# Kernel tuning notes

Hardware: AMD Instinct MI355X
Metric: run time of the kernel (lower is better)

The kernel has to match this reference:

```python
import jax, jax.numpy as jnp
import numpy as np

B, S, H = 4, 2048, 1024
NH, HD = 16, 64


def setup_inputs() -> dict:
    key = jax.random.key(0)
    ks = jax.random.split(key, 5)
    scale = 1.0 / np.sqrt(H)
    x = jax.random.normal(ks[0], (B, S, H), dtype=jnp.float32)
    w_qkv = jax.random.normal(ks[1], (H, 3 * H), dtype=jnp.float32) * scale
    b_qkv = jnp.zeros((3 * H,), dtype=jnp.float32)
    w_out = jax.random.normal(ks[2], (H, H), dtype=jnp.float32) * scale
    b_out = jnp.zeros((H,), dtype=jnp.float32)
    return {"x": x, "w_qkv": w_qkv, "b_qkv": b_qkv, "w_out": w_out, "b_out": b_out}


def reference(x, w_qkv, b_qkv, w_out, b_out):
    bsz, seq_len, hidden = x.shape
    qkv = x @ w_qkv + b_qkv  # [B,S,3H]
    q, k, v = jnp.split(qkv, 3, axis=-1)

    def heads(t):
        return t.reshape(bsz, seq_len, NH, HD).transpose(0, 2, 1, 3)  # [B,NH,S,HD]

    q, k, v = heads(q), heads(k), heads(v)
    scale = HD ** (-0.5)
    attn = jnp.einsum("bhqd,bhkd->bhqk", q, k) * scale  # [B,NH,S,S]
    causal = jnp.tril(jnp.ones((seq_len, seq_len), dtype=bool))
    attn = jnp.where(causal, attn, -jnp.inf)
    probs = jax.nn.softmax(attn, axis=-1)
    out = jnp.einsum("bhqk,bhkd->bhqd", probs, v)
    out = out.transpose(0, 2, 1, 3).reshape(bsz, seq_len, hidden)
    return out @ w_out + b_out
```

## Files before the change

### kernel.cpp

```cpp
#include <hip/hip_runtime.h>
#include <hip/hip_bf16.h>
#include <cstdint>

#define B_  4
#define S_  2048
#define H_  1024
#define NH_ 16
#define HD_ 64

using short8  = __attribute__((ext_vector_type(8))) short;
using floatx4 = __attribute__((ext_vector_type(4))) float;

__device__ __forceinline__ unsigned short f2b(float f) {
  union { float f; unsigned int u; } x; x.f = f;
  unsigned int r = x.u + 0x7fffu + ((x.u >> 16) & 1u);
  return (unsigned short)(r >> 16);
}
__device__ __forceinline__ unsigned short f2b_fast(float f) {
  union { float f; unsigned int u; } x; x.f = f;
  return (unsigned short)((x.u + 0x8000u) >> 16);
}
__device__ __forceinline__ unsigned int pack2(float a, float b) {
  return (unsigned int)f2b(a) | ((unsigned int)f2b(b) << 16);
}

__device__ __forceinline__ void async16(void* lds, const void* g) {
  __builtin_amdgcn_global_load_lds(
      (const __attribute__((address_space(1))) unsigned int*)g,
      (__attribute__((address_space(3))) unsigned int*)lds, 16, 0, 0);
}

__device__ __forceinline__ void transpose_tile(const float* __restrict__ in,
                                               unsigned short* __restrict__ out,
                                               int R, int C, int c0, int r0) {
  __shared__ float tile[32][33];
  int tx = threadIdx.x & 31, ty = threadIdx.x >> 5;
  for (int i = 0; i < 4; i++) {
    int r = r0 + ty + i * 8;
    tile[ty + i * 8][tx] = in[(size_t)r * C + c0 + tx];
  }
  __syncthreads();
  for (int i = 0; i < 4; i++) {
    int c = c0 + ty + i * 8;
    out[(size_t)c * R + r0 + tx] = f2b(tile[tx][ty + i * 8]);
  }
}

__global__ void k_prep(const float* __restrict__ x, const float* __restrict__ w_qkv,
                       const float* __restrict__ w_out,
                       unsigned short* __restrict__ xb, unsigned short* __restrict__ wqkvT,
                       unsigned short* __restrict__ woutT) {
  int bx = blockIdx.x;
  if (bx < 8192) {
    int i = (bx * 256 + threadIdx.x) * 4;
    float4 v = *(const float4*)(x + i);
    ushort4 o;
    o.x = f2b(v.x); o.y = f2b(v.y); o.z = f2b(v.z); o.w = f2b(v.w);
    *(ushort4*)(xb + i) = o;
  } else if (bx < 8192 + 3072) {
    int t = bx - 8192;
    transpose_tile(w_qkv, wqkvT, H_, 3 * H_, (t % 96) * 32, (t / 96) * 32);
  } else {
    int t = bx - 8192 - 3072;
    transpose_tile(w_out, woutT, H_, H_, (t & 31) * 32, (t >> 5) * 32);
  }
}

template <bool OUT_BF16>
__global__ __launch_bounds__(256, 2) void k_gemm_wide(
    const unsigned short* __restrict__ A,
    const unsigned short* __restrict__ BT,
    const float* __restrict__ bias,
    void* __restrict__ Cout,
    unsigned short* __restrict__ vt,
    int M, int N, int K) {
  __shared__ __align__(16) unsigned short As[2][128 * 32];
  __shared__ __align__(16) unsigned short Bs[2][256 * 32];
  const int tid  = threadIdx.x;
  const int lane = tid & 63, wave = tid >> 6;
  const int quad = lane >> 4, l16 = lane & 15;
  const int wm = wave >> 1, wn = wave & 1;
  const int m0 = blockIdx.y * 128, n0 = blockIdx.x * 256;

  floatx4 acc[4][8];
#pragma unroll
  for (int mt = 0; mt < 4; mt++)
#pragma unroll
    for (int nt = 0; nt < 8; nt++)
      acc[mt][nt] = (floatx4){0.f, 0.f, 0.f, 0.f};

  auto stage = [&](int k0, int bufi) {
#pragma unroll
    for (int j = 0; j < 6; j++) {
      int g = wave * 384 + j * 64 + lane;
      if (g < 512) {
        int row = g >> 2, c8 = (g & 3) ^ ((row >> 1) & 3);
        async16(&As[bufi][g * 8], &A[(size_t)(m0 + row) * K + k0 + c8 * 8]);
      } else {
        int c = g - 512;
        int row = c >> 2, c8 = (c & 3) ^ ((row >> 1) & 3);
        async16(&Bs[bufi][c * 8], &BT[(size_t)(n0 + row) * K + k0 + c8 * 8]);
      }
    }
  };

  stage(0, 0);
  int it = 0;
  for (int k0 = 0; k0 < K; k0 += 32, it++) {
    const int cur = it & 1;
    __syncthreads();
    if (k0 + 32 < K) stage(k0 + 32, cur ^ 1);

    short8 af[4];
#pragma unroll
    for (int t = 0; t < 4; t++) {
      int ra = wm * 64 + t * 16 + l16;
      af[t] = *(const short8*)&As[cur][(ra * 4 + (quad ^ ((ra >> 1) & 3))) * 8];
    }
#pragma unroll
    for (int h = 0; h < 2; h++) {
      short8 bq[4];
#pragma unroll
      for (int t = 0; t < 4; t++) {
        int rb = wn * 128 + (h * 4 + t) * 16 + l16;
        bq[t] = *(const short8*)&Bs[cur][(rb * 4 + (quad ^ ((rb >> 1) & 3))) * 8];
      }
#pragma unroll
      for (int mt = 0; mt < 4; mt++)
#pragma unroll
        for (int nt = 0; nt < 4; nt++)
          acc[mt][h * 4 + nt] =
              __builtin_amdgcn_mfma_f32_16x16x32_bf16(af[mt], bq[nt], acc[mt][h * 4 + nt], 0, 0, 0);
    }
  }

  if (OUT_BF16 && n0 >= 2048) {
#pragma unroll
    for (int mt = 0; mt < 4; mt++) {
      int row0 = m0 + wm * 64 + mt * 16 + quad * 4;
      int b = row0 >> 11, s = row0 & 2047;
#pragma unroll
      for (int nt = 0; nt < 8; nt++) {
        int col = n0 + wn * 128 + nt * 16 + l16;
        float bv = bias[col];
        uint2 u;
        u.x = pack2(acc[mt][nt][0] + bv, acc[mt][nt][1] + bv);
        u.y = pack2(acc[mt][nt][2] + bv, acc[mt][nt][3] + bv);
        *(uint2*)&vt[(size_t)(b * 1024 + (col - 2048)) * S_ + s] = u;
      }
    }
  } else {
#pragma unroll
    for (int mt = 0; mt < 4; mt++) {
      int row = m0 + wm * 64 + mt * 16 + quad * 4;
#pragma unroll
      for (int nt = 0; nt < 8; nt++) {
        int col = n0 + wn * 128 + nt * 16 + l16;
        float bv = bias[col];
#pragma unroll
        for (int r = 0; r < 4; r++) {
          float v = acc[mt][nt][r] + bv;
          if (OUT_BF16) ((unsigned short*)Cout)[(size_t)(row + r) * N + col] = f2b(v);
          else          ((float*)Cout)[(size_t)(row + r) * N + col] = v;
        }
      }
    }
  }
}

template <bool OUT_BF16>
__global__ __launch_bounds__(256, 4) void k_gemm_bt(
    const unsigned short* __restrict__ A,
    const unsigned short* __restrict__ BT,
    const float* __restrict__ bias,
    void* __restrict__ Cout,
    unsigned short* __restrict__ vt,
    int M, int N, int K) {
  __shared__ __align__(16) unsigned short As[2][128 * 32];
  __shared__ __align__(16) unsigned short Bs[2][128 * 32];
  const int tid  = threadIdx.x;
  const int lane = tid & 63, wave = tid >> 6;
  const int quad = lane >> 4, l16 = lane & 15;
  const int wm = wave >> 1, wn = wave & 1;
  const int m0 = blockIdx.y * 128, n0 = blockIdx.x * 128;
  const int wv2 = wave & 1;

  const unsigned short* srcbase = (wave < 2) ? A : BT;
  const int base0 = (wave < 2) ? m0 : n0;

  floatx4 acc[4][4];
  for (int mt = 0; mt < 4; mt++)
    for (int nt = 0; nt < 4; nt++)
      acc[mt][nt] = (floatx4){0.f, 0.f, 0.f, 0.f};

  auto stage = [&](int k0, int bufi) {
    unsigned short* dst = (wave < 2) ? &As[bufi][0] : &Bs[bufi][0];
    for (int j = 0; j < 4; j++) {
      int c = wv2 * 256 + j * 64 + lane;
      int row = c >> 2, slot = c & 3;
      int c8 = slot ^ ((row >> 1) & 3);
      async16(&dst[c * 8], &srcbase[(size_t)(base0 + row) * K + k0 + c8 * 8]);
    }
  };

  stage(0, 0);
  int it = 0;
  for (int k0 = 0; k0 < K; k0 += 32, it++) {
    const int cur = it & 1;
    __syncthreads();
    if (k0 + 32 < K) stage(k0 + 32, cur ^ 1);
    short8 af[4], bq[4];
    for (int t = 0; t < 4; t++) {
      int ra = wm * 64 + t * 16 + l16;
      int rb = wn * 64 + t * 16 + l16;
      af[t] = *(const short8*)&As[cur][(ra * 4 + (quad ^ ((ra >> 1) & 3))) * 8];
      bq[t] = *(const short8*)&Bs[cur][(rb * 4 + (quad ^ ((rb >> 1) & 3))) * 8];
    }
    for (int mt = 0; mt < 4; mt++)
      for (int nt = 0; nt < 4; nt++)
        acc[mt][nt] = __builtin_amdgcn_mfma_f32_16x16x32_bf16(af[mt], bq[nt], acc[mt][nt], 0, 0, 0);
  }

  if (OUT_BF16 && n0 >= 2048) {
    for (int mt = 0; mt < 4; mt++) {
      int row0 = m0 + wm * 64 + mt * 16 + quad * 4;
      int b = row0 >> 11, s = row0 & 2047;
      for (int nt = 0; nt < 4; nt++) {
        int col = n0 + wn * 64 + nt * 16 + l16;
        float bv = bias[col];
        uint2 u;
        u.x = pack2(acc[mt][nt][0] + bv, acc[mt][nt][1] + bv);
        u.y = pack2(acc[mt][nt][2] + bv, acc[mt][nt][3] + bv);
        *(uint2*)&vt[(size_t)(b * 1024 + (col - 2048)) * S_ + s] = u;
      }
    }
  } else {
    for (int mt = 0; mt < 4; mt++) {
      int row = m0 + wm * 64 + mt * 16 + quad * 4;
      for (int nt = 0; nt < 4; nt++) {
        int col = n0 + wn * 64 + nt * 16 + l16;
        float bv = bias[col];
        for (int r = 0; r < 4; r++) {
          float v = acc[mt][nt][r] + bv;
          if (OUT_BF16) ((unsigned short*)Cout)[(size_t)(row + r) * N + col] = f2b(v);
          else          ((float*)Cout)[(size_t)(row + r) * N + col] = v;
        }
      }
    }
  }
}

__global__ __launch_bounds__(256, 3) void k_attn(
    const unsigned short* __restrict__ qkv,
    const unsigned short* __restrict__ vt,
    unsigned short* __restrict__ outb) {
  __shared__ __align__(16) unsigned short Ks [2][64 * 64];
  __shared__ __align__(16) unsigned short VTs[2][64 * 64];
  __shared__ __align__(16) unsigned short Ps[4][16 * 64];

  const int tid  = threadIdx.x;
  const int lane = tid & 63, w = tid >> 6;
  const int quad = lane >> 4, l16 = lane & 15;
  const int qt = (S_ / 128 - 1) - (blockIdx.x >> 6);
  const int bh = blockIdx.x & 63;
  const int b = bh >> 4, h = bh & 15;
  const int qwv = qt * 128 + w * 32;
  const int wv2 = w & 1;

  short8 qf[2][2];
  for (int g = 0; g < 2; g++)
    for (int kh = 0; kh < 2; kh++)
      qf[g][kh] = *(const short8*)&qkv[(size_t)(b * S_ + qwv + g * 16 + l16) * (3 * H_)
                                       + h * HD_ + kh * 32 + quad * 8];

  floatx4 oacc[2][4];
  float lsum[2] = {0.f, 0.f};
  for (int g = 0; g < 2; g++)
    for (int ct = 0; ct < 4; ct++) oacc[g][ct] = (floatx4){0.f, 0.f, 0.f, 0.f};

  auto stage = [&](int kt, int bufi) {
    if (w < 2) {
      for (int j = 0; j < 4; j++) {
        int c = wv2 * 256 + j * 64 + lane;
        int row = c >> 3, c8 = (c & 7) ^ (row & 7);
        async16(&Ks[bufi][c * 8],
                &qkv[(size_t)(b * S_ + kt * 64 + row) * (3 * H_) + H_ + h * HD_ + c8 * 8]);
      }
    } else {
      for (int j = 0; j < 4; j++) {
        int c = wv2 * 256 + j * 64 + lane;
        int row = c >> 3, c8 = (c & 7) ^ (row & 7);
        async16(&VTs[bufi][c * 8],
                &vt[(size_t)(bh * HD_ + row) * S_ + kt * 64 + c8 * 8]);
      }
    }
  };

  unsigned short* Pw = &Ps[w][0];

  const int ktmax = 2 * qt + 1;
  stage(0, 0);
  for (int kt = 0; kt <= ktmax; kt++) {
    const int cur = kt & 1;
    __syncthreads();
    if (kt < ktmax) stage(kt + 1, cur ^ 1);

    if (kt * 64 <= qwv + 31) {
      const bool need_mask = (kt * 64 + 63 > qwv);

      short8 vf[4][2];
      for (int ct = 0; ct < 4; ct++)
        for (int kh = 0; kh < 2; kh++) {
          int vrow = ct * 16 + l16;
          vf[ct][kh] = *(const short8*)&VTs[cur][(vrow * 8 + ((kh * 4 + quad) ^ (vrow & 7))) * 8];
        }

      uint2 pk[2][4];
      for (int ct = 0; ct < 4; ct++) {
        int krow = ct * 16 + l16;
        short8 kf0 = *(const short8*)&Ks[cur][(krow * 8 + ((0 + quad) ^ (krow & 7))) * 8];
        short8 kf1 = *(const short8*)&Ks[cur][(krow * 8 + ((4 + quad) ^ (krow & 7))) * 8];
        for (int g = 0; g < 2; g++) {
          floatx4 z = (floatx4){0.f, 0.f, 0.f, 0.f};
          z = __builtin_amdgcn_mfma_f32_16x16x32_bf16(kf0, qf[g][0], z, 0, 0, 0);
          z = __builtin_amdgcn_mfma_f32_16x16x32_bf16(kf1, qf[g][1], z, 0, 0, 0);
          float p[4];
          if (need_mask) {
            int kvb = kt * 64 + ct * 16 + quad * 4;
            int q = qwv + g * 16 + l16;
            for (int r = 0; r < 4; r++)
              p[r] = (kvb + r <= q) ? __expf(z[r] * 0.125f) : 0.f;
          } else {
            for (int r = 0; r < 4; r++) p[r] = __expf(z[r] * 0.125f);
          }
          lsum[g] += (p[0] + p[1]) + (p[2] + p[3]);
          pk[g][ct].x = (unsigned int)f2b_fast(p[0]) | ((unsigned int)f2b_fast(p[1]) << 16);
          pk[g][ct].y = (unsigned int)f2b_fast(p[2]) | ((unsigned int)f2b_fast(p[3]) << 16);
        }
      }

      for (int g = 0; g < 2; g++) {
        for (int ct = 0; ct < 4; ct++) {
          int slot = (ct * 2 + (quad >> 1)) ^ (l16 & 7);
          *(uint2*)&Pw[l16 * 64 + slot * 8 + (quad & 1) * 4] = pk[g][ct];
        }
        for (int kh = 0; kh < 2; kh++) {
          short8 pf = *(const short8*)&Pw[l16 * 64 + ((kh * 4 + quad) ^ (l16 & 7)) * 8];
          for (int ct = 0; ct < 4; ct++)
            oacc[g][ct] = __builtin_amdgcn_mfma_f32_16x16x32_bf16(vf[ct][kh], pf, oacc[g][ct], 0, 0, 0);
        }
      }
    }
  }

  for (int g = 0; g < 2; g++) {
    lsum[g] += __shfl_xor(lsum[g], 16);
    lsum[g] += __shfl_xor(lsum[g], 32);
  }

  for (int g = 0; g < 2; g++) {
    float inv = 1.0f / lsum[g];
    int q = qwv + g * 16 + l16;
    for (int ct = 0; ct < 4; ct++) {
      uint2 u;
      u.x = pack2(oacc[g][ct][0] * inv, oacc[g][ct][1] * inv);
      u.y = pack2(oacc[g][ct][2] * inv, oacc[g][ct][3] * inv);
      *(uint2*)&outb[(size_t)(b * S_ + q) * H_ + h * HD_ + ct * 16 + quad * 4] = u;
    }
  }
}

extern "C" void kernel_launch(void* const* d_in, const int* in_sizes, int n_in,
                              void* d_out, int out_size, void* d_ws, size_t ws_size,
                              hipStream_t stream) {
  const float* x     = (const float*)d_in[0];
  const float* w_qkv = (const float*)d_in[1];
  const float* b_qkv = (const float*)d_in[2];
  const float* w_out = (const float*)d_in[3];
  const float* b_out = (const float*)d_in[4];

  char* ws = (char*)d_ws;
  size_t off = 0;
  auto alloc = [&](size_t bytes) -> void* {
    void* p = ws + off;
    off = (off + bytes + 255) & ~(size_t)255;
    return p;
  };
  unsigned short* xb    = (unsigned short*)alloc((size_t)B_ * S_ * H_ * 2);
  unsigned short* wqkvT = (unsigned short*)alloc((size_t)3 * H_ * H_ * 2);
  unsigned short* woutT = (unsigned short*)alloc((size_t)H_ * H_ * 2);
  unsigned short* qkv   = (unsigned short*)alloc((size_t)B_ * S_ * 3 * H_ * 2);
  unsigned short* ao    = (unsigned short*)alloc((size_t)B_ * S_ * H_ * 2);
  unsigned short* vtb   = (unsigned short*)alloc((size_t)B_ * NH_ * HD_ * S_ * 2);

  k_prep<<<8192 + 3072 + 1024, 256, 0, stream>>>(x, w_qkv, w_out, xb, wqkvT, woutT);

  k_gemm_wide<true ><<<dim3(3 * H_ / 256, B_ * S_ / 128), 256, 0, stream>>>(
      xb, wqkvT, b_qkv, qkv, vtb, B_ * S_, 3 * H_, H_);

  k_attn<<<(S_ / 128) * 64, 256, 0, stream>>>(qkv, vtb, ao);

  k_gemm_bt<false><<<dim3(H_ / 128, B_ * S_ / 128), 256, 0, stream>>>(
      ao, woutT, b_out, (float*)d_out, nullptr, B_ * S_, H_, H_);
}
```

Before: 249.1 us.

## Fold softmax scale into Q weights, retile QKV GEMM to 128x128xK64, prioritize PV MFMA

```diff
diff --git a/kernel.cpp b/kernel.cpp
--- a/kernel.cpp
+++ b/kernel.cpp
@@ -32,7 +32,8 @@
 
 __device__ __forceinline__ void transpose_tile(const float* __restrict__ in,
                                                unsigned short* __restrict__ out,
-                                               int R, int C, int c0, int r0) {
+                                               int R, int C, int c0, int r0,
+                                               bool qk_scale) {
   __shared__ float tile[32][33];
   int tx = threadIdx.x & 31, ty = threadIdx.x >> 5;
   for (int i = 0; i < 4; i++) {
@@ -42,7 +43,8 @@
   __syncthreads();
   for (int i = 0; i < 4; i++) {
     int c = c0 + ty + i * 8;
-    out[(size_t)c * R + r0 + tx] = f2b(tile[tx][ty + i * 8]);
+    float s = (qk_scale && c < 1024) ? 0.125f : 1.0f;
+    out[(size_t)c * R + r0 + tx] = f2b(tile[tx][ty + i * 8] * s);
   }
 }
 
@@ -59,79 +61,75 @@
     *(ushort4*)(xb + i) = o;
   } else if (bx < 8192 + 3072) {
     int t = bx - 8192;
-    transpose_tile(w_qkv, wqkvT, H_, 3 * H_, (t % 96) * 32, (t / 96) * 32);
+    transpose_tile(w_qkv, wqkvT, H_, 3 * H_, (t % 96) * 32, (t / 96) * 32, true);
   } else {
     int t = bx - 8192 - 3072;
-    transpose_tile(w_out, woutT, H_, H_, (t & 31) * 32, (t >> 5) * 32);
+    transpose_tile(w_out, woutT, H_, H_, (t & 31) * 32, (t >> 5) * 32, false);
   }
 }
 
 template <bool OUT_BF16>
-__global__ __launch_bounds__(256, 2) void k_gemm_wide(
+__global__ __launch_bounds__(256, 2) void k_gemm_bt64(
     const unsigned short* __restrict__ A,
     const unsigned short* __restrict__ BT,
     const float* __restrict__ bias,
     void* __restrict__ Cout,
     unsigned short* __restrict__ vt,
     int M, int N, int K) {
-  __shared__ __align__(16) unsigned short As[2][128 * 32];
-  __shared__ __align__(16) unsigned short Bs[2][256 * 32];
+  __shared__ __align__(16) unsigned short As[2][128 * 64];
+  __shared__ __align__(16) unsigned short Bs[2][128 * 64];
   const int tid  = threadIdx.x;
   const int lane = tid & 63, wave = tid >> 6;
   const int quad = lane >> 4, l16 = lane & 15;
   const int wm = wave >> 1, wn = wave & 1;
-  const int m0 = blockIdx.y * 128, n0 = blockIdx.x * 256;
-
-  floatx4 acc[4][8];
+  const int m0 = blockIdx.y * 128, n0 = blockIdx.x * 128;
+
+  floatx4 acc[4][4];
 #pragma unroll
   for (int mt = 0; mt < 4; mt++)
 #pragma unroll
-    for (int nt = 0; nt < 8; nt++)
+    for (int nt = 0; nt < 4; nt++)
       acc[mt][nt] = (floatx4){0.f, 0.f, 0.f, 0.f};
 
   auto stage = [&](int k0, int bufi) {
 #pragma unroll
-    for (int j = 0; j < 6; j++) {
-      int g = wave * 384 + j * 64 + lane;
-      if (g < 512) {
-        int row = g >> 2, c8 = (g & 3) ^ ((row >> 1) & 3);
-        async16(&As[bufi][g * 8], &A[(size_t)(m0 + row) * K + k0 + c8 * 8]);
-      } else {
-        int c = g - 512;
-        int row = c >> 2, c8 = (c & 3) ^ ((row >> 1) & 3);
-        async16(&Bs[bufi][c * 8], &BT[(size_t)(n0 + row) * K + k0 + c8 * 8]);
-      }
+    for (int j = 0; j < 4; j++) {
+      int c = j * 256 + tid;
+      int row = c >> 3, c8 = (c & 7) ^ (row & 7);
+      async16(&As[bufi][c * 8], &A[(size_t)(m0 + row) * K + k0 + c8 * 8]);
+    }
+#pragma unroll
+    for (int j = 0; j < 4; j++) {
+      int c = j * 256 + tid;
+      int row = c >> 3, c8 = (c & 7) ^ (row & 7);
+      async16(&Bs[bufi][c * 8], &BT[(size_t)(n0 + row) * K + k0 + c8 * 8]);
     }
   };
 
   stage(0, 0);
   int it = 0;
-  for (int k0 = 0; k0 < K; k0 += 32, it++) {
+  for (int k0 = 0; k0 < K; k0 += 64, it++) {
     const int cur = it & 1;
     __syncthreads();
-    if (k0 + 32 < K) stage(k0 + 32, cur ^ 1);
-
-    short8 af[4];
+    if (k0 + 64 < K) stage(k0 + 64, cur ^ 1);
+    short8 af[4][2], bq[4][2];
 #pragma unroll
     for (int t = 0; t < 4; t++) {
       int ra = wm * 64 + t * 16 + l16;
-      af[t] = *(const short8*)&As[cur][(ra * 4 + (quad ^ ((ra >> 1) & 3))) * 8];
-    }
-#pragma unroll
-    for (int h = 0; h < 2; h++) {
-      short8 bq[4];
-#pragma unroll
-      for (int t = 0; t < 4; t++) {
-        int rb = wn * 128 + (h * 4 + t) * 16 + l16;
-        bq[t] = *(const short8*)&Bs[cur][(rb * 4 + (quad ^ ((rb >> 1) & 3))) * 8];
-      }
+      int rb = wn * 64 + t * 16 + l16;
+#pragma unroll
+      for (int ks = 0; ks < 2; ks++) {
+        af[t][ks] = *(const short8*)&As[cur][(ra * 8 + ((ks * 4 + quad) ^ (ra & 7))) * 8];
+        bq[t][ks] = *(const short8*)&Bs[cur][(rb * 8 + ((ks * 4 + quad) ^ (rb & 7))) * 8];
+      }
+    }
+#pragma unroll
+    for (int ks = 0; ks < 2; ks++)
 #pragma unroll
       for (int mt = 0; mt < 4; mt++)
 #pragma unroll
         for (int nt = 0; nt < 4; nt++)
-          acc[mt][h * 4 + nt] =
-              __builtin_amdgcn_mfma_f32_16x16x32_bf16(af[mt], bq[nt], acc[mt][h * 4 + nt], 0, 0, 0);
-    }
+          acc[mt][nt] = __builtin_amdgcn_mfma_f32_16x16x32_bf16(af[mt][ks], bq[nt][ks], acc[mt][nt], 0, 0, 0);
   }
 
   if (OUT_BF16 && n0 >= 2048) {
@@ -140,8 +138,8 @@
       int row0 = m0 + wm * 64 + mt * 16 + quad * 4;
       int b = row0 >> 11, s = row0 & 2047;
 #pragma unroll
-      for (int nt = 0; nt < 8; nt++) {
-        int col = n0 + wn * 128 + nt * 16 + l16;
+      for (int nt = 0; nt < 4; nt++) {
+        int col = n0 + wn * 64 + nt * 16 + l16;
         float bv = bias[col];
         uint2 u;
         u.x = pack2(acc[mt][nt][0] + bv, acc[mt][nt][1] + bv);
@@ -154,9 +152,10 @@
     for (int mt = 0; mt < 4; mt++) {
       int row = m0 + wm * 64 + mt * 16 + quad * 4;
 #pragma unroll
-      for (int nt = 0; nt < 8; nt++) {
-        int col = n0 + wn * 128 + nt * 16 + l16;
+      for (int nt = 0; nt < 4; nt++) {
+        int col = n0 + wn * 64 + nt * 16 + l16;
         float bv = bias[col];
+        if (OUT_BF16 && col < 1024) bv *= 0.125f;
 #pragma unroll
         for (int r = 0; r < 4; r++) {
           float v = acc[mt][nt][r] + bv;
@@ -329,9 +328,9 @@
             int kvb = kt * 64 + ct * 16 + quad * 4;
             int q = qwv + g * 16 + l16;
             for (int r = 0; r < 4; r++)
-              p[r] = (kvb + r <= q) ? __expf(z[r] * 0.125f) : 0.f;
+              p[r] = (kvb + r <= q) ? __expf(z[r]) : 0.f;
           } else {
-            for (int r = 0; r < 4; r++) p[r] = __expf(z[r] * 0.125f);
+            for (int r = 0; r < 4; r++) p[r] = __expf(z[r]);
           }
           lsum[g] += (p[0] + p[1]) + (p[2] + p[3]);
           pk[g][ct].x = (unsigned int)f2b_fast(p[0]) | ((unsigned int)f2b_fast(p[1]) << 16);
@@ -346,8 +345,10 @@
         }
         for (int kh = 0; kh < 2; kh++) {
           short8 pf = *(const short8*)&Pw[l16 * 64 + ((kh * 4 + quad) ^ (l16 & 7)) * 8];
+          __builtin_amdgcn_s_setprio(1);
           for (int ct = 0; ct < 4; ct++)
             oacc[g][ct] = __builtin_amdgcn_mfma_f32_16x16x32_bf16(vf[ct][kh], pf, oacc[g][ct], 0, 0, 0);
+          __builtin_amdgcn_s_setprio(0);
         }
       }
     }
@@ -395,7 +396,7 @@
 
   k_prep<<<8192 + 3072 + 1024, 256, 0, stream>>>(x, w_qkv, w_out, xb, wqkvT, woutT);
 
-  k_gemm_wide<true ><<<dim3(3 * H_ / 256, B_ * S_ / 128), 256, 0, stream>>>(
+  k_gemm_bt64<true ><<<dim3(3 * H_ / 128, B_ * S_ / 128), 256, 0, stream>>>(
       xb, wqkvT, b_qkv, qkv, vtb, B_ * S_, 3 * H_, H_);
 
   k_attn<<<(S_ / 128) * 64, 256, 0, stream>>>(qkv, vtb, ao);
```

After: 244.5 us. About the same (-1.8%).
